# Kernel optimization log

Hardware: AMD Instinct MI355X
Metric: run time of the kernel (lower is better)

The kernel has to match this reference:

```python
import jax, jax.numpy as jnp
import numpy as np

LMAX, RB, RA, N, D = 4, 12, 11, 131072, 64
S = (LMAX + 1) ** 2


def _assoc_legendre_norm(lmax, x):
    # Fully-normalized associated Legendre P_l^m(x), orthonormal over the sphere
    # (includes sqrt((2l+1)/(4pi) * (l-m)!/(l+m)!)). x: [B] = cos(beta).
    B = x.shape[0]
    s = np.sqrt(np.clip(1.0 - x * x, 0.0, 1.0))
    P = np.zeros((lmax + 1, lmax + 1, B))
    P[0, 0] = np.sqrt(1.0 / (4.0 * np.pi))
    for m in range(1, lmax + 1):
        P[m, m] = -np.sqrt((2.0 * m + 1.0) / (2.0 * m)) * s * P[m - 1, m - 1]
    for m in range(0, lmax):
        P[m + 1, m] = np.sqrt(2.0 * m + 3.0) * x * P[m, m]
    for m in range(0, lmax + 1):
        for l in range(m + 2, lmax + 1):
            a = np.sqrt((4.0 * l * l - 1.0) / (l * l - m * m))
            b = np.sqrt((((l - 1) ** 2 - m * m)) / (4.0 * (l - 1) ** 2 - 1.0))
            P[l, m] = a * (x * P[l - 1, m] - b * P[l - 2, m])
    return P


def _sh_grid(lmax, res_beta, res_alpha):
    # Real orthonormal spherical harmonics sampled on a Gauss-Legendre x uniform-alpha grid,
    # plus quadrature weights so that sum_{b,a} Y_i Y_j qw_b = delta_ij (band-limited).
    x, w = np.polynomial.legendre.leggauss(res_beta)  # nodes in cos(beta)
    alpha = 2.0 * np.pi * np.arange(res_alpha) / res_alpha
    P = _assoc_legendre_norm(lmax, x)  # [L+1, L+1, RB]
    Ssz = (lmax + 1) ** 2
    Y = np.zeros((res_beta, res_alpha, Ssz))
    i = 0
    for l in range(lmax + 1):
        for m in range(-l, l + 1):
            if m < 0:
                ang = np.sqrt(2.0) * np.sin(-m * alpha)
            elif m == 0:
                ang = np.ones_like(alpha)
            else:
                ang = np.sqrt(2.0) * np.cos(m * alpha)
            Y[:, :, i] = P[l, abs(m)][:, None] * ang[None, :]
            i += 1
    qw = w * (2.0 * np.pi / res_alpha)  # beta quadrature * alpha trapezoid weight
    return Y.astype(np.float32), qw.astype(np.float32)


def setup_inputs() -> dict:
    key = jax.random.key(0)
    k1, k2, k3, k4 = jax.random.split(key, 4)
    Y_np, qw_np = _sh_grid(LMAX, RB, RA)
    Y = jnp.asarray(Y_np)                       # [RB, RA, S]
    Yw = Y * jnp.asarray(qw_np)[:, None, None]  # [RB, RA, S] (quadrature-weighted)
    input1 = jax.random.normal(k1, (N, D), dtype=jnp.float32)
    input2 = jax.random.normal(k2, (N, D), dtype=jnp.float32)
    W1 = jax.random.normal(k3, (D, S), dtype=jnp.float32) * 0.1
    W2 = jax.random.normal(k4, (D, S), dtype=jnp.float32) * 0.1
    return {"input1": input1, "input2": input2, "W1": W1, "W2": W2, "Y": Y, "Yw": Yw}


def reference(input1, input2, W1, W2, Y, Yw):
    # linear_in: project input irreps to S2 spherical-harmonic coefficients
    c1 = input1 @ W1  # [N, S]
    c2 = input2 @ W2  # [N, S]
    # ToS2Grid: evaluate band-limited signal on the (beta, alpha) grid
    g1 = jnp.einsum("ns,bas->nba", c1, Y)  # [N, RB, RA]
    g2 = jnp.einsum("ns,bas->nba", c2, Y)
    # pointwise product on the sphere, then FromS2Grid (quadrature projection)
    return jnp.einsum("nba,bas->ns", g1 * g2, Yw)  # [N, S]
```

## Files before the change

### kernel.cpp

```cpp
#include <hip/hip_runtime.h>


typedef _Float16 f16x8 __attribute__((ext_vector_type(8)));
typedef _Float16 f16x4 __attribute__((ext_vector_type(4)));
typedef float f32x4 __attribute__((ext_vector_type(4)));
typedef float f32x4u __attribute__((ext_vector_type(4), aligned(4)));

namespace {
constexpr int kD = 64, kS = 25, kP = 132;
constexpr int kBlock = 256, kM = 256;
constexpr int kWsA2 = 9216, kWsYw = 18432;
}

__global__ void precompute_kernel(const float* __restrict__ W1,
                                  const float* __restrict__ W2,
                                  const float* __restrict__ Y,
                                  const float* __restrict__ Yw,
                                  _Float16* __restrict__ ws) {
    const int t0 = blockIdx.x * blockDim.x + threadIdx.x;
    const int stride = gridDim.x * blockDim.x;
    for (int e = t0; e < 9216; e += stride) {
        const int j = e & 7, lane = (e >> 3) & 63, ks = (e >> 9) & 1, pt = e >> 10;
        const int d = ks * 32 + (lane >> 4) * 8 + j;
        const int p = pt * 16 + (lane & 15);
        float v1 = 0.f, v2 = 0.f;
        if (p < kP) {
            const float* yr = Y + p * kS;
            const float* w1 = W1 + d * kS;
            const float* w2 = W2 + d * kS;
            #pragma unroll
            for (int s = 0; s < kS; ++s) {
                v1 = fmaf(w1[s], yr[s], v1);
                v2 = fmaf(w2[s], yr[s], v2);
            }
        }
        ws[e]         = (_Float16)v1;
        ws[kWsA2 + e] = (_Float16)v2;
    }
    for (int e = t0; e < 4608; e += stride) {
        const int i = e & 3, lane = (e >> 2) & 63, r = e >> 8;
        const int pt = r % 9, st = r / 9;
        const int p = pt * 16 + ((lane >> 4) & 3) * 4 + i;
        const int s = st * 16 + (lane & 15);
        ws[kWsYw + e] = (s < kS && p < kP) ? (_Float16)Yw[p * kS + s]
                                           : (_Float16)0.f;
    }
}

__device__ __forceinline__ f16x8 ld8(const _Float16* p) {
    return *reinterpret_cast<const f16x8*>(p);
}
__device__ __forceinline__ f16x4 ld4(const _Float16* p) {
    return *reinterpret_cast<const f16x4*>(p);
}
__device__ __forceinline__ f16x8 cvt8h(f32x4 u, f32x4 v) {
    f16x8 r;
    r[0] = (_Float16)u[0]; r[1] = (_Float16)u[1];
    r[2] = (_Float16)u[2]; r[3] = (_Float16)u[3];
    r[4] = (_Float16)v[0]; r[5] = (_Float16)v[1];
    r[6] = (_Float16)v[2]; r[7] = (_Float16)v[3];
    return r;
}

__global__ __launch_bounds__(kBlock, 3) void gaunt_mfma7(
    const float* __restrict__ in1, const float* __restrict__ in2,
    const _Float16* __restrict__ ws, float* __restrict__ out)
{
    const int tid  = threadIdx.x;
    const int lane = tid & 63;
    const int w    = __builtin_amdgcn_readfirstlane(tid >> 6);
    const int lo16 = lane & 15, quad = lane >> 4;

    const long long base = (long long)blockIdx.x * (kM * kD);
    f16x8 b1[4][2], b2[4][2];
    #pragma unroll
    for (int rt = 0; rt < 4; ++rt) {
        const int row = (4 * w + rt) * 16 + lo16;
        const float* p1 = in1 + base + row * kD + quad * 8;
        const float* p2 = in2 + base + row * kD + quad * 8;
        #pragma unroll
        for (int ks = 0; ks < 2; ++ks) {
            const f32x4 u1 = *reinterpret_cast<const f32x4*>(p1 + ks * 32);
            const f32x4 v1 = *reinterpret_cast<const f32x4*>(p1 + ks * 32 + 4);
            const f32x4 u2 = *reinterpret_cast<const f32x4*>(p2 + ks * 32);
            const f32x4 v2 = *reinterpret_cast<const f32x4*>(p2 + ks * 32 + 4);
            b1[rt][ks] = cvt8h(u1, v1);
            b2[rt][ks] = cvt8h(u2, v2);
        }
    }

    const _Float16* wsA1 = ws;
    const _Float16* wsA2 = ws + kWsA2;
    const _Float16* wsYw = ws + kWsYw;

    f32x4 oacc[4][2];
    #pragma unroll
    for (int rt = 0; rt < 4; ++rt)
        #pragma unroll
        for (int st = 0; st < 2; ++st)
            oacc[rt][st] = (f32x4){0.f, 0.f, 0.f, 0.f};

    f16x8 a1c[2], a2c[2], a1n[2], a2n[2];
    f16x4 ywc[2], ywn[2];
    #pragma unroll
    for (int ks = 0; ks < 2; ++ks) {
        a1c[ks] = ld8(&wsA1[ks * 512 + lane * 8]);
        a2c[ks] = ld8(&wsA2[ks * 512 + lane * 8]);
    }
    #pragma unroll
    for (int st = 0; st < 2; ++st)
        ywc[st] = ld4(&wsYw[(st * 9) * 256 + lane * 4]);

    #pragma unroll 1
    for (int pt = 0; pt < 9; ++pt) {
        if (pt < 8) {
            #pragma unroll
            for (int ks = 0; ks < 2; ++ks) {
                a1n[ks] = ld8(&wsA1[((pt + 1) * 2 + ks) * 512 + lane * 8]);
                a2n[ks] = ld8(&wsA2[((pt + 1) * 2 + ks) * 512 + lane * 8]);
            }
            #pragma unroll
            for (int st = 0; st < 2; ++st)
                ywn[st] = ld4(&wsYw[(st * 9 + pt + 1) * 256 + lane * 4]);
        }
        #pragma unroll
        for (int rt = 0; rt < 4; ++rt) {
            f32x4 g1 = (f32x4){0.f, 0.f, 0.f, 0.f};
            f32x4 g2 = (f32x4){0.f, 0.f, 0.f, 0.f};
            #pragma unroll
            for (int ks = 0; ks < 2; ++ks) {
                g1 = __builtin_amdgcn_mfma_f32_16x16x32_f16(a1c[ks], b1[rt][ks], g1, 0, 0, 0);
                g2 = __builtin_amdgcn_mfma_f32_16x16x32_f16(a2c[ks], b2[rt][ks], g2, 0, 0, 0);
            }
            f16x4 h;
            h[0] = (_Float16)(g1[0] * g2[0]);
            h[1] = (_Float16)(g1[1] * g2[1]);
            h[2] = (_Float16)(g1[2] * g2[2]);
            h[3] = (_Float16)(g1[3] * g2[3]);
            #pragma unroll
            for (int st = 0; st < 2; ++st)
                oacc[rt][st] = __builtin_amdgcn_mfma_f32_16x16x16f16(
                    ywc[st], h, oacc[rt][st], 0, 0, 0);
        }
        #pragma unroll
        for (int ks = 0; ks < 2; ++ks) { a1c[ks] = a1n[ks]; a2c[ks] = a2n[ks]; }
        ywc[0] = ywn[0]; ywc[1] = ywn[1];
    }

    const long long ob = (long long)blockIdx.x * (kM * kS);
    #pragma unroll
    for (int rt = 0; rt < 4; ++rt) {
        const int row = (4 * w + rt) * 16 + lo16;
        float* rp = out + ob + (long long)row * kS;
        *reinterpret_cast<f32x4u*>(rp + quad * 4) = oacc[rt][0];
        if (quad < 2) {
            *reinterpret_cast<f32x4u*>(rp + 16 + quad * 4) = oacc[rt][1];
        } else if (quad == 2) {
            rp[24] = oacc[rt][1][0];
        }
    }
}

extern "C" void kernel_launch(void* const* d_in, const int* in_sizes, int n_in,
                              void* d_out, int out_size, void* d_ws, size_t ws_size,
                              hipStream_t stream) {
    const float* in1 = (const float*)d_in[0];
    const float* in2 = (const float*)d_in[1];
    const float* W1  = (const float*)d_in[2];
    const float* W2  = (const float*)d_in[3];
    const float* Y   = (const float*)d_in[4];
    const float* Yw  = (const float*)d_in[5];
    float* out = (float*)d_out;
    _Float16* ws = (_Float16*)d_ws;

    precompute_kernel<<<64, 256, 0, stream>>>(W1, W2, Y, Yw, ws);

    const int n_rows = in_sizes[0] / kD;
    const int grid = n_rows / kM;
    gaunt_mfma7<<<grid, kBlock, 0, stream>>>(in1, in2, ws, out);
}
```

Measured before the change: 113.6 us.

## Fuse precompute into main kernel and restructure grid evaluation via SH coefficients

Removes the separate precompute kernel. Each block now stages Y (fp16) and Yw fragments in LDS and loads W1/W2 into registers. Instead of using the precomputed W·Y product matrix, it first computes c = input·W with MFMA and transposes the result through an LDS scratch. It then evaluates the grid as Y·c, which needs one MFMA per grid tile in place of two. The cost is per-block prologue work (global loads of W, Y and Yw, plus LDS staging and a sync), more LDS use, and occupancy lowered from 3 to 2 in launch bounds.

New measurement: 114.5 us. No clear change (+0.8%).

```diff
diff --git a/kernel.cpp b/kernel.cpp
--- a/kernel.cpp
+++ b/kernel.cpp
@@ -9,42 +9,11 @@
 namespace {
 constexpr int kD = 64, kS = 25, kP = 132;
 constexpr int kBlock = 256, kM = 256;
-constexpr int kWsA2 = 9216, kWsYw = 18432;
-}
-
-__global__ void precompute_kernel(const float* __restrict__ W1,
-                                  const float* __restrict__ W2,
-                                  const float* __restrict__ Y,
-                                  const float* __restrict__ Yw,
-                                  _Float16* __restrict__ ws) {
-    const int t0 = blockIdx.x * blockDim.x + threadIdx.x;
-    const int stride = gridDim.x * blockDim.x;
-    for (int e = t0; e < 9216; e += stride) {
-        const int j = e & 7, lane = (e >> 3) & 63, ks = (e >> 9) & 1, pt = e >> 10;
-        const int d = ks * 32 + (lane >> 4) * 8 + j;
-        const int p = pt * 16 + (lane & 15);
-        float v1 = 0.f, v2 = 0.f;
-        if (p < kP) {
-            const float* yr = Y + p * kS;
-            const float* w1 = W1 + d * kS;
-            const float* w2 = W2 + d * kS;
-            #pragma unroll
-            for (int s = 0; s < kS; ++s) {
-                v1 = fmaf(w1[s], yr[s], v1);
-                v2 = fmaf(w2[s], yr[s], v2);
-            }
-        }
-        ws[e]         = (_Float16)v1;
-        ws[kWsA2 + e] = (_Float16)v2;
-    }
-    for (int e = t0; e < 4608; e += stride) {
-        const int i = e & 3, lane = (e >> 2) & 63, r = e >> 8;
-        const int pt = r % 9, st = r / 9;
-        const int p = pt * 16 + ((lane >> 4) & 3) * 4 + i;
-        const int s = st * 16 + (lane & 15);
-        ws[kWsYw + e] = (s < kS && p < kP) ? (_Float16)Yw[p * kS + s]
-                                           : (_Float16)0.f;
-    }
+constexpr int kYfOff  = 0;
+constexpr int kYwOff  = 4608;
+constexpr int kScrOff = 9216;
+constexpr int kScrRow = 48;
+constexpr int kLdsHalfs = 15360;
 }
 
 __device__ __forceinline__ f16x8 ld8(const _Float16* p) {
@@ -62,14 +31,74 @@
     return r;
 }
 
-__global__ __launch_bounds__(kBlock, 3) void gaunt_mfma7(
+__global__ __launch_bounds__(kBlock, 2) void gaunt_fused8(
     const float* __restrict__ in1, const float* __restrict__ in2,
-    const _Float16* __restrict__ ws, float* __restrict__ out)
+    const float* __restrict__ W1, const float* __restrict__ W2,
+    const float* __restrict__ Y,  const float* __restrict__ Yw,
+    float* __restrict__ out)
 {
+    __shared__ _Float16 lds[kLdsHalfs];
     const int tid  = threadIdx.x;
     const int lane = tid & 63;
     const int w    = __builtin_amdgcn_readfirstlane(tid >> 6);
     const int lo16 = lane & 15, quad = lane >> 4;
+
+    for (int pair = tid; pair < 576; pair += kBlock) {
+        const int pt = pair >> 6;
+        const int ln = pair & 63;
+        const int p  = pt * 16 + (ln & 15);
+        const int s0 = ((ln >> 4) & 3) * 8;
+        f16x8 v;
+        #pragma unroll
+        for (int j = 0; j < 8; ++j) v[j] = (_Float16)0.f;
+        if (p < kP) {
+            const float* yp = Y + p * kS + s0;
+            if (s0 < 24) {
+                const f32x4u u = *reinterpret_cast<const f32x4u*>(yp);
+                const f32x4u q = *reinterpret_cast<const f32x4u*>(yp + 4);
+                #pragma unroll
+                for (int j = 0; j < 4; ++j) {
+                    v[j]     = (_Float16)u[j];
+                    v[4 + j] = (_Float16)q[j];
+                }
+            } else {
+                v[0] = (_Float16)yp[0];
+            }
+        }
+        *reinterpret_cast<f16x8*>(&lds[kYfOff + (pt * 64 + ln) * 8]) = v;
+    }
+
+    for (int e = tid; e < 4608; e += kBlock) {
+        const int i = e & 3, ln = (e >> 2) & 63, r = e >> 8;
+        const int pt = r % 9, st = r / 9;
+        const int p = pt * 16 + ((ln >> 4) & 3) * 4 + i;
+        const int s = st * 16 + (ln & 15);
+        lds[kYwOff + e] = (s < kS && p < kP) ? (_Float16)Yw[p * kS + s]
+                                             : (_Float16)0.f;
+    }
+
+    f16x8 w1f[2][2], w2f[2][2];
+    #pragma unroll
+    for (int st = 0; st < 2; ++st) {
+        const int s = st * 16 + lo16;
+        #pragma unroll
+        for (int ks = 0; ks < 2; ++ks) {
+            f16x8 a, b;
+            #pragma unroll
+            for (int j = 0; j < 8; ++j) { a[j] = (_Float16)0.f; b[j] = (_Float16)0.f; }
+            if (s < kS) {
+                const int d0 = ks * 32 + quad * 8;
+                #pragma unroll
+                for (int j = 0; j < 8; ++j) {
+                    a[j] = (_Float16)W1[(d0 + j) * kS + s];
+                    b[j] = (_Float16)W2[(d0 + j) * kS + s];
+                }
+            }
+            w1f[st][ks] = a; w2f[st][ks] = b;
+        }
+    }
+
+    __syncthreads();
 
     const long long base = (long long)blockIdx.x * (kM * kD);
     f16x8 b1[4][2], b2[4][2];
@@ -89,9 +118,33 @@
         }
     }
 
-    const _Float16* wsA1 = ws;
-    const _Float16* wsA2 = ws + kWsA2;
-    const _Float16* wsYw = ws + kWsYw;
+    f16x8 c1t[4], c2t[4];
+    _Float16* scr = &lds[kScrOff + w * (2 * 16 * kScrRow)];
+    #pragma unroll
+    for (int rt = 0; rt < 4; ++rt) {
+        f32x4 c1[2], c2[2];
+        #pragma unroll
+        for (int st = 0; st < 2; ++st) {
+            c1[st] = (f32x4){0.f, 0.f, 0.f, 0.f};
+            c2[st] = (f32x4){0.f, 0.f, 0.f, 0.f};
+        }
+        #pragma unroll
+        for (int st = 0; st < 2; ++st)
+            #pragma unroll
+            for (int ks = 0; ks < 2; ++ks) {
+                c1[st] = __builtin_amdgcn_mfma_f32_16x16x32_f16(b1[rt][ks], w1f[st][ks], c1[st], 0, 0, 0);
+                c2[st] = __builtin_amdgcn_mfma_f32_16x16x32_f16(b2[rt][ks], w2f[st][ks], c2[st], 0, 0, 0);
+            }
+        #pragma unroll
+        for (int st = 0; st < 2; ++st)
+            #pragma unroll
+            for (int i = 0; i < 4; ++i) {
+                scr[(quad * 4 + i) * kScrRow + st * 16 + lo16]       = (_Float16)c1[st][i];
+                scr[768 + (quad * 4 + i) * kScrRow + st * 16 + lo16] = (_Float16)c2[st][i];
+            }
+        c1t[rt] = ld8(&scr[lo16 * kScrRow + quad * 8]);
+        c2t[rt] = ld8(&scr[768 + lo16 * kScrRow + quad * 8]);
+    }
 
     f32x4 oacc[4][2];
     #pragma unroll
@@ -100,51 +153,32 @@
         for (int st = 0; st < 2; ++st)
             oacc[rt][st] = (f32x4){0.f, 0.f, 0.f, 0.f};
 
-    f16x8 a1c[2], a2c[2], a1n[2], a2n[2];
-    f16x4 ywc[2], ywn[2];
-    #pragma unroll
-    for (int ks = 0; ks < 2; ++ks) {
-        a1c[ks] = ld8(&wsA1[ks * 512 + lane * 8]);
-        a2c[ks] = ld8(&wsA2[ks * 512 + lane * 8]);
-    }
-    #pragma unroll
-    for (int st = 0; st < 2; ++st)
-        ywc[st] = ld4(&wsYw[(st * 9) * 256 + lane * 4]);
+    f16x8 yc  = ld8(&lds[kYfOff + lane * 8]);
+    f16x4 yw0 = ld4(&lds[kYwOff + lane * 4]);
+    f16x4 yw1 = ld4(&lds[kYwOff + 9 * 256 + lane * 4]);
 
     #pragma unroll 1
     for (int pt = 0; pt < 9; ++pt) {
+        f16x8 yn; f16x4 yw0n, yw1n;
         if (pt < 8) {
-            #pragma unroll
-            for (int ks = 0; ks < 2; ++ks) {
-                a1n[ks] = ld8(&wsA1[((pt + 1) * 2 + ks) * 512 + lane * 8]);
-                a2n[ks] = ld8(&wsA2[((pt + 1) * 2 + ks) * 512 + lane * 8]);
-            }
-            #pragma unroll
-            for (int st = 0; st < 2; ++st)
-                ywn[st] = ld4(&wsYw[(st * 9 + pt + 1) * 256 + lane * 4]);
+            yn   = ld8(&lds[kYfOff + (pt + 1) * 512 + lane * 8]);
+            yw0n = ld4(&lds[kYwOff + (pt + 1) * 256 + lane * 4]);
+            yw1n = ld4(&lds[kYwOff + (9 + pt + 1) * 256 + lane * 4]);
         }
         #pragma unroll
         for (int rt = 0; rt < 4; ++rt) {
-            f32x4 g1 = (f32x4){0.f, 0.f, 0.f, 0.f};
-            f32x4 g2 = (f32x4){0.f, 0.f, 0.f, 0.f};
-            #pragma unroll
-            for (int ks = 0; ks < 2; ++ks) {
-                g1 = __builtin_amdgcn_mfma_f32_16x16x32_f16(a1c[ks], b1[rt][ks], g1, 0, 0, 0);
-                g2 = __builtin_amdgcn_mfma_f32_16x16x32_f16(a2c[ks], b2[rt][ks], g2, 0, 0, 0);
-            }
+            f32x4 z = (f32x4){0.f, 0.f, 0.f, 0.f};
+            f32x4 g1 = __builtin_amdgcn_mfma_f32_16x16x32_f16(yc, c1t[rt], z, 0, 0, 0);
+            f32x4 g2 = __builtin_amdgcn_mfma_f32_16x16x32_f16(yc, c2t[rt], z, 0, 0, 0);
             f16x4 h;
             h[0] = (_Float16)(g1[0] * g2[0]);
             h[1] = (_Float16)(g1[1] * g2[1]);
             h[2] = (_Float16)(g1[2] * g2[2]);
             h[3] = (_Float16)(g1[3] * g2[3]);
-            #pragma unroll
-            for (int st = 0; st < 2; ++st)
-                oacc[rt][st] = __builtin_amdgcn_mfma_f32_16x16x16f16(
-                    ywc[st], h, oacc[rt][st], 0, 0, 0);
-        }
-        #pragma unroll
-        for (int ks = 0; ks < 2; ++ks) { a1c[ks] = a1n[ks]; a2c[ks] = a2n[ks]; }
-        ywc[0] = ywn[0]; ywc[1] = ywn[1];
+            oacc[rt][0] = __builtin_amdgcn_mfma_f32_16x16x16f16(yw0, h, oacc[rt][0], 0, 0, 0);
+            oacc[rt][1] = __builtin_amdgcn_mfma_f32_16x16x16f16(yw1, h, oacc[rt][1], 0, 0, 0);
+        }
+        yc = yn; yw0 = yw0n; yw1 = yw1n;
     }
 
     const long long ob = (long long)blockIdx.x * (kM * kS);
@@ -171,11 +205,9 @@
     const float* Y   = (const float*)d_in[4];
     const float* Yw  = (const float*)d_in[5];
     float* out = (float*)d_out;
-    _Float16* ws = (_Float16*)d_ws;
-
-    precompute_kernel<<<64, 256, 0, stream>>>(W1, W2, Y, Yw, ws);
+    (void)d_ws; (void)ws_size;
 
     const int n_rows = in_sizes[0] / kD;
     const int grid = n_rows / kM;
-    gaunt_mfma7<<<grid, kBlock, 0, stream>>>(in1, in2, ws, out);
-}
+    gaunt_fused8<<<grid, kBlock, 0, stream>>>(in1, in2, W1, W2, Y, Yw, out);
+}
```
